# Kernel tuning notes

Measured on AMD Instinct MI355X. Metric: run time of the kernel, lower is better.

Reference implementation:

```python
import jax, jax.numpy as jnp
import numpy as np

GAMMA = 0.5
BATCH, DIM, UNITS = 16384, 512, 1024


def setup_inputs() -> dict:
    key = jax.random.key(0)
    k1, k2 = jax.random.split(key)
    inputs = jax.random.normal(k1, (BATCH, DIM), dtype=jnp.float32)
    mu = jax.random.normal(k2, (DIM, UNITS), dtype=jnp.float32)
    return {"inputs": inputs, "mu": mu}


def reference(inputs, mu):
    # Squared L2 distance from each input row to each center (column of mu):
    x_sq = jnp.sum(inputs * inputs, axis=1, keepdims=True)        # [B, 1]
    mu_sq = jnp.sum(mu * mu, axis=0, keepdims=True)               # [1, U]
    cross = inputs @ mu                                           # [B, U] GEMM
    l2 = x_sq - 2.0 * cross + mu_sq                                # [B, U]
    return jnp.exp(-GAMMA * l2)
```

## Files before the change

### kernel.cpp

```cpp
#include <hip/hip_runtime.h>
#include <hip/hip_bf16.h>

#define BATCH 16384
#define DIM   512
#define UNITS 1024

typedef float v16f __attribute__((ext_vector_type(16)));

#define BPITCH 33
#define FPITCH 520

__global__ __launch_bounds__(256)
void prep_b_kernel(const float* __restrict__ mu, unsigned char* __restrict__ B8f,
                   float* __restrict__ musq) {
    __shared__ __attribute__((aligned(16))) char smem[512 * BPITCH * 4 + 1024];
    float* lds = (float*)smem;
    float* red = (float*)(smem + 512 * BPITCH * 4);
    const int t  = threadIdx.x;
    const int l  = t & 63, w = t >> 6;
    const int ln = l & 31, h = l >> 5;
    const int nb = blockIdx.x;
    const int n0 = nb * 32;
    const int col = t & 31, kg = t >> 5;
    float s = 0.f;
    for (int i = 0; i < 64; i++) {
        const int k = i * 8 + kg;
        float v = mu[(size_t)k * UNITS + n0 + col];
        s += v * v;
        lds[k * BPITCH + col] = v;
    }
    red[col * 8 + kg] = s;
    __syncthreads();
    if (t < 32) {
        float a = 0.f;
#pragma unroll
        for (int i = 0; i < 8; i++) a += red[t * 8 + i];
        musq[n0 + t] = a;
    }
#pragma unroll
    for (int j = 0; j < 8; j++) {
        const int kw = w * 8 + j;
        const float* p = lds + (kw * 16 + h * 8) * BPITCH + ln;
        float f[8];
#pragma unroll
        for (int i = 0; i < 8; i++) f[i] = p[i * BPITCH];
        int lo = __builtin_amdgcn_cvt_pk_fp8_f32(f[0], f[1], 0, false);
        lo     = __builtin_amdgcn_cvt_pk_fp8_f32(f[2], f[3], lo, true);
        int hi = __builtin_amdgcn_cvt_pk_fp8_f32(f[4], f[5], 0, false);
        hi     = __builtin_amdgcn_cvt_pk_fp8_f32(f[6], f[7], hi, true);
        *(int2*)(B8f + (((size_t)nb * 32 + kw) * 64 + l) * 8) = make_int2(lo, hi);
    }
}

__global__ __launch_bounds__(512, 4)
void rbf_fused_kernel(const float* __restrict__ in,
                      const unsigned char* __restrict__ B8f,
                      const float* __restrict__ musq,
                      float* __restrict__ out) {
    __shared__ __attribute__((aligned(16))) char smem[32 * FPITCH + 256];
    unsigned char* Af = (unsigned char*)smem;
    float* red = (float*)(smem + 32 * FPITCH);

    const int t  = threadIdx.x;
    const int l  = t & 63;
    const int w  = t >> 6;
    const int ln = l & 31;
    const int h  = l >> 5;
    const int m0 = blockIdx.x * 32;

    const float4* src = (const float4*)(in + (size_t)m0 * DIM);
#pragma unroll
    for (int i = 0; i < 8; i++) {
        const int f = i * 512 + t;
        float4 v = src[f];
        float ss = v.x * v.x + v.y * v.y + v.z * v.z + v.w * v.w;
        int p = __builtin_amdgcn_cvt_pk_fp8_f32(v.x, v.y, 0, false);
        p     = __builtin_amdgcn_cvt_pk_fp8_f32(v.z, v.w, p, true);
        *(int*)(Af + (f >> 7) * FPITCH + (f & 127) * 4) = p;
        for (int off = 32; off; off >>= 1) ss += __shfl_down(ss, off, 64);
        if (l == 0) red[(i * 4 + (w >> 1)) * 2 + (w & 1)] = ss;
    }
    __syncthreads();

    const int n0 = w * 128;
    const long* bptr = (const long*)B8f + (size_t)(n0 >> 5) * 2048 + l;
    const unsigned char* ap = Af + ln * FPITCH + h * 8;

    v16f acc[4];
#pragma unroll
    for (int g = 0; g < 4; g++) acc[g] = (v16f)0.f;

#pragma unroll 4
    for (int kw = 0; kw < 32; kw++) {
        long a  = *(const long*)(ap + kw * 16);
        long b0 = bptr[kw * 64];
        long b1 = bptr[2048 + kw * 64];
        long b2 = bptr[4096 + kw * 64];
        long b3 = bptr[6144 + kw * 64];
        acc[0] = __builtin_amdgcn_mfma_f32_32x32x16_fp8_fp8(a, b0, acc[0], 0, 0, 0);
        acc[1] = __builtin_amdgcn_mfma_f32_32x32x16_fp8_fp8(a, b1, acc[1], 0, 0, 0);
        acc[2] = __builtin_amdgcn_mfma_f32_32x32x16_fp8_fp8(a, b2, acc[2], 0, 0, 0);
        acc[3] = __builtin_amdgcn_mfma_f32_32x32x16_fp8_fp8(a, b3, acc[3], 0, 0, 0);
    }

    const float xv = -0.5f * (red[ln * 2] + red[ln * 2 + 1]);
#pragma unroll
    for (int g = 0; g < 4; g++) {
        const int nc = n0 + g * 32;
        const float mb = -0.5f * musq[nc + ln];
#pragma unroll
        for (int r = 0; r < 16; r++) {
            const int rl = (r & 3) + 8 * (r >> 2) + 4 * h;
            const float xb = __shfl(xv, rl, 64);
            float v = __expf(acc[g][r] + xb + mb);
            __builtin_nontemporal_store(
                v, out + (size_t)(m0 + rl) * UNITS + nc + ln);
        }
    }
}

extern "C" void kernel_launch(void* const* d_in, const int* in_sizes, int n_in,
                              void* d_out, int out_size, void* d_ws, size_t ws_size,
                              hipStream_t stream) {
    const float* inputs = (const float*)d_in[0];
    const float* mu     = (const float*)d_in[1];
    float* out = (float*)d_out;

    char* ws = (char*)d_ws;
    unsigned char* B8f = (unsigned char*)ws;
    float* musq        = (float*)(ws + (size_t)UNITS * DIM);

    prep_b_kernel<<<UNITS / 32, 256, 0, stream>>>(mu, B8f, musq);
    rbf_fused_kernel<<<BATCH / 32, 512, 0, stream>>>(inputs, B8f, musq, out);
}
```

Measured before the change: 122.9 us.

## Retile RBF kernel into 128x128 output tiles with 2x2 warp MFMA blocking

Each block previously covered 32 rows against all 1024 units using 8 waves, so every A fragment fed four MFMAs while each B fragment was used once per load. Now each 256-thread block computes a 128x128 output tile. Each wave computes a 64x64 sub-tile, so every loaded A and B fragment is reused twice. The block index is swizzled so that groups of blocks share input rows. The trade-off is that each input row is now read and converted to fp8 eight times, once per column tile, instead of once.

```diff
diff --git a/kernel.cpp b/kernel.cpp
--- a/kernel.cpp
+++ b/kernel.cpp
@@ -8,7 +8,7 @@
 typedef float v16f __attribute__((ext_vector_type(16)));
 
 #define BPITCH 33
-#define FPITCH 520
+#define APITCH 520
 
 __global__ __launch_bounds__(256)
 void prep_b_kernel(const float* __restrict__ mu, unsigned char* __restrict__ B8f,
@@ -52,69 +52,86 @@
     }
 }
 
-__global__ __launch_bounds__(512, 4)
+__global__ __launch_bounds__(256, 4)
 void rbf_fused_kernel(const float* __restrict__ in,
                       const unsigned char* __restrict__ B8f,
                       const float* __restrict__ musq,
                       float* __restrict__ out) {
-    __shared__ __attribute__((aligned(16))) char smem[32 * FPITCH + 256];
-    unsigned char* Af = (unsigned char*)smem;
-    float* red = (float*)(smem + 32 * FPITCH);
+    __shared__ __attribute__((aligned(16))) char smem[128 * APITCH + 512];
+    unsigned char* A8 = (unsigned char*)smem;
+    float* xsql = (float*)(smem + 128 * APITCH);
 
     const int t  = threadIdx.x;
     const int l  = t & 63;
     const int w  = t >> 6;
     const int ln = l & 31;
     const int h  = l >> 5;
-    const int m0 = blockIdx.x * 32;
 
-    const float4* src = (const float4*)(in + (size_t)m0 * DIM);
-#pragma unroll
-    for (int i = 0; i < 8; i++) {
-        const int f = i * 512 + t;
-        float4 v = src[f];
-        float ss = v.x * v.x + v.y * v.y + v.z * v.z + v.w * v.w;
-        int p = __builtin_amdgcn_cvt_pk_fp8_f32(v.x, v.y, 0, false);
-        p     = __builtin_amdgcn_cvt_pk_fp8_f32(v.z, v.w, p, true);
-        *(int*)(Af + (f >> 7) * FPITCH + (f & 127) * 4) = p;
+    const int b  = blockIdx.x;
+    const int x  = b & 7;
+    const int j  = b >> 3;
+    const int m0 = (x * 16 + (j >> 3)) * 128;
+    const int n0 = (j & 7) * 128;
+
+    const int rbase = w * 32;
+    const float4* asrc = (const float4*)(in + (size_t)(m0 + rbase) * DIM);
+#pragma unroll 4
+    for (int rr = 0; rr < 32; rr++) {
+        float4 u = asrc[rr * 128 + l];
+        float4 v = asrc[rr * 128 + 64 + l];
+        float ss = u.x * u.x + u.y * u.y + u.z * u.z + u.w * u.w
+                 + v.x * v.x + v.y * v.y + v.z * v.z + v.w * v.w;
+        int pu = __builtin_amdgcn_cvt_pk_fp8_f32(u.x, u.y, 0, false);
+        pu     = __builtin_amdgcn_cvt_pk_fp8_f32(u.z, u.w, pu, true);
+        int pv = __builtin_amdgcn_cvt_pk_fp8_f32(v.x, v.y, 0, false);
+        pv     = __builtin_amdgcn_cvt_pk_fp8_f32(v.z, v.w, pv, true);
+        *(int*)(A8 + (rbase + rr) * APITCH + l * 4)       = pu;
+        *(int*)(A8 + (rbase + rr) * APITCH + 256 + l * 4) = pv;
         for (int off = 32; off; off >>= 1) ss += __shfl_down(ss, off, 64);
-        if (l == 0) red[(i * 4 + (w >> 1)) * 2 + (w & 1)] = ss;
+        if (l == 0) xsql[rbase + rr] = ss;
     }
     __syncthreads();
 
-    const int n0 = w * 128;
-    const long* bptr = (const long*)B8f + (size_t)(n0 >> 5) * 2048 + l;
-    const unsigned char* ap = Af + ln * FPITCH + h * 8;
+    const int wm = (w >> 1) * 64;
+    const int wn = (w & 1) * 64;
+    const long* Bf = (const long*)B8f + (size_t)((n0 + wn) >> 5) * 2048 + l;
+    const unsigned char* Ab0 = A8 + (wm + ln) * APITCH + h * 8;
+    const unsigned char* Ab1 = Ab0 + 32 * APITCH;
 
-    v16f acc[4];
+    v16f acc[2][2];
 #pragma unroll
-    for (int g = 0; g < 4; g++) acc[g] = (v16f)0.f;
+    for (int c = 0; c < 2; c++)
+#pragma unroll
+        for (int g = 0; g < 2; g++) acc[c][g] = (v16f)0.f;
 
 #pragma unroll 4
     for (int kw = 0; kw < 32; kw++) {
-        long a  = *(const long*)(ap + kw * 16);
-        long b0 = bptr[kw * 64];
-        long b1 = bptr[2048 + kw * 64];
-        long b2 = bptr[4096 + kw * 64];
-        long b3 = bptr[6144 + kw * 64];
-        acc[0] = __builtin_amdgcn_mfma_f32_32x32x16_fp8_fp8(a, b0, acc[0], 0, 0, 0);
-        acc[1] = __builtin_amdgcn_mfma_f32_32x32x16_fp8_fp8(a, b1, acc[1], 0, 0, 0);
-        acc[2] = __builtin_amdgcn_mfma_f32_32x32x16_fp8_fp8(a, b2, acc[2], 0, 0, 0);
-        acc[3] = __builtin_amdgcn_mfma_f32_32x32x16_fp8_fp8(a, b3, acc[3], 0, 0, 0);
+        long a0 = *(const long*)(Ab0 + kw * 16);
+        long a1 = *(const long*)(Ab1 + kw * 16);
+        long b0 = Bf[kw * 64];
+        long b1 = Bf[2048 + kw * 64];
+        acc[0][0] = __builtin_amdgcn_mfma_f32_32x32x16_fp8_fp8(a0, b0, acc[0][0], 0, 0, 0);
+        acc[0][1] = __builtin_amdgcn_mfma_f32_32x32x16_fp8_fp8(a0, b1, acc[0][1], 0, 0, 0);
+        acc[1][0] = __builtin_amdgcn_mfma_f32_32x32x16_fp8_fp8(a1, b0, acc[1][0], 0, 0, 0);
+        acc[1][1] = __builtin_amdgcn_mfma_f32_32x32x16_fp8_fp8(a1, b1, acc[1][1], 0, 0, 0);
     }
 
-    const float xv = -0.5f * (red[ln * 2] + red[ln * 2 + 1]);
 #pragma unroll
-    for (int g = 0; g < 4; g++) {
-        const int nc = n0 + g * 32;
-        const float mb = -0.5f * musq[nc + ln];
+    for (int c = 0; c < 2; c++) {
+        const int mc = wm + c * 32;
+        const float xv = -0.5f * xsql[mc + ln];
 #pragma unroll
-        for (int r = 0; r < 16; r++) {
-            const int rl = (r & 3) + 8 * (r >> 2) + 4 * h;
-            const float xb = __shfl(xv, rl, 64);
-            float v = __expf(acc[g][r] + xb + mb);
-            __builtin_nontemporal_store(
-                v, out + (size_t)(m0 + rl) * UNITS + nc + ln);
+        for (int g = 0; g < 2; g++) {
+            const int nc = n0 + wn + g * 32;
+            const float mb = -0.5f * musq[nc + ln];
+#pragma unroll
+            for (int r = 0; r < 16; r++) {
+                const int rl = (r & 3) + 8 * (r >> 2) + 4 * h;
+                const float xb = __shfl(xv, rl, 64);
+                float v = __expf(acc[c][g][r] + xb + mb);
+                __builtin_nontemporal_store(
+                    v, out + (size_t)(m0 + mc + rl) * UNITS + nc + ln);
+            }
         }
     }
 }
@@ -131,5 +148,5 @@
     float* musq        = (float*)(ws + (size_t)UNITS * DIM);
 
     prep_b_kernel<<<UNITS / 32, 256, 0, stream>>>(mu, B8f, musq);
-    rbf_fused_kernel<<<BATCH / 32, 512, 0, stream>>>(inputs, B8f, musq, out);
+    rbf_fused_kernel<<<1024, 256, 0, stream>>>(inputs, B8f, musq, out);
 }
```

Result: slower. 144.5 us (+17.6%).
